# Kernel optimization log

Hardware: AMD Instinct MI355X
Metric: run time of the kernel (lower is better)

The kernel has to match this reference:

```python
import jax, jax.numpy as jnp
import numpy as np

N, R, IN, OUT = 16384, 64, 128, 128


def setup_inputs() -> dict:
    key = jax.random.key(0)
    k1, k2, k3, k4 = jax.random.split(key, 4)
    x = jax.random.normal(k1, (N, IN), dtype=jnp.float32)
    relations = jax.random.randint(k2, (N, 1), 0, R, dtype=jnp.int32)
    # kaiming_uniform_(a=sqrt(5)) on [R, in, out] -> bound = 1/sqrt(fan_in); bias uses same bound
    bound = 1.0 / np.sqrt(IN)
    w = jax.random.uniform(k3, (R, IN, OUT), dtype=jnp.float32, minval=-bound, maxval=bound)
    bias = jax.random.uniform(k4, (R, OUT), dtype=jnp.float32, minval=-bound, maxval=bound)
    return {"x": x, "relations": relations, "w": w, "bias": bias}


def reference(x, relations, w, bias):
    # Faithful math of the torch module: out[i] = x[i] @ w[relations[i,0]] + bias[relations[i,0]]
    # (original computes x.matmul(w[relations]) -> [N,1,N,out] and extracts the diagonal;
    #  this is the direct per-sample grouped GEMM form.)
    rel = relations[:, 0]                       # [N]
    w_sel = jnp.take(w, rel, axis=0)            # [N, in, out]
    out = jnp.einsum('ni,nio->no', x, w_sel)    # [N, out]
    return out + jnp.take(bias, rel, axis=0)
```

## Files before the change

### kernel.cpp

```cpp
#include <hip/hip_runtime.h>

#define N_ROWS 16384
#define R_REL  64
#define IN_D   128
#define OUT_D  128
#define BM     64
#define NS     4
#define TPB_G  256

__device__ __forceinline__ float f4c(const float4& v, int i) {
  return i == 0 ? v.x : i == 1 ? v.y : i == 2 ? v.z : v.w;
}

__global__ __launch_bounds__(256, 4) void k_pre(const int* __restrict__ rel,
                                                int* __restrict__ offsets,
                                                int* __restrict__ row_idx) {
  const int r = blockIdx.x;
  const int t = threadIdx.x;
  const int wid = t >> 6, lane = t & 63;
  __shared__ int wsum[4];
  __shared__ int sbase;
  const int4* rel4 = (const int4*)rel;

  int lt = 0;
  for (int i = t; i < N_ROWS / 4; i += 256) {
    const int4 v = rel4[i];
    lt += (v.x < r) + (v.y < r) + (v.z < r) + (v.w < r);
  }
  #pragma unroll
  for (int d = 32; d >= 1; d >>= 1) lt += __shfl_down(lt, d, 64);
  if (lane == 0) wsum[wid] = lt;
  __syncthreads();
  if (t == 0) {
    const int o = wsum[0] + wsum[1] + wsum[2] + wsum[3];
    sbase = o;
    offsets[r] = o;
    if (r == R_REL - 1) offsets[R_REL] = N_ROWS;
  }
  __syncthreads();
  int base = sbase;

  for (int c = 0; c < 16; ++c) {
    const int i4 = c * 256 + t;
    const int4 v = rel4[i4];
    const int m0 = (v.x == r), m1 = (v.y == r), m2 = (v.z == r), m3 = (v.w == r);
    const int cnt_t = m0 + m1 + m2 + m3;
    int incl = cnt_t;
    #pragma unroll
    for (int d = 1; d < 64; d <<= 1) {
      const int u = __shfl_up(incl, d, 64);
      if (lane >= d) incl += u;
    }
    if (lane == 63) wsum[wid] = incl;
    __syncthreads();
    int wbase = 0;
    for (int ww = 0; ww < wid; ++ww) wbase += wsum[ww];
    int pos = base + wbase + incl - cnt_t;
    const int row0 = i4 * 4;
    if (m0) row_idx[pos++] = row0;
    if (m1) row_idx[pos++] = row0 + 1;
    if (m2) row_idx[pos++] = row0 + 2;
    if (m3) row_idx[pos++] = row0 + 3;
    base += wsum[0] + wsum[1] + wsum[2] + wsum[3];
    __syncthreads();
  }
}

__global__ __launch_bounds__(TPB_G, 2) void k_gemm(const float* __restrict__ x,
                                                   const float* __restrict__ w,
                                                   const float* __restrict__ bias,
                                                   const int* __restrict__ offsets,
                                                   const int* __restrict__ row_idx,
                                                   float* __restrict__ out) {
  __shared__ __align__(16) float ws_[IN_D * 64];
  __shared__ __align__(16) float xs[BM * IN_D];
  const int r = blockIdx.y;
  const int c0 = blockIdx.z * 64;
  const int beg = offsets[r];
  const int cnt = offsets[r + 1] - beg;
  if (cnt == 0) return;
  const int t = threadIdx.x;
  const int tx = t & 15;
  const int ty = t >> 4;

  {
    const float* wr = w + (size_t)r * (IN_D * OUT_D) + c0;
    #pragma unroll
    for (int i = 0; i < 8; ++i) {
      const int id = t + i * 256;
      const int k = id >> 4, c4 = id & 15;
      ((float4*)ws_)[k * 16 + c4] = *(const float4*)(wr + k * OUT_D + c4 * 4);
    }
  }

  for (int tile = blockIdx.x; tile * BM < cnt; tile += NS) {
    const int m0 = beg + tile * BM;
    const int rows = min(BM, cnt - tile * BM);

    {
      const int row = t & 63;
      const int q = t >> 6;
      if (row < rows) {
        const int g = row_idx[m0 + row];
        const float4* src = (const float4*)(x + (size_t)g * IN_D) + q * 8;
        float4* dst = (float4*)xs + row * 32;
        const int sw = row & 7;
        #pragma unroll
        for (int j = 0; j < 8; ++j) dst[(q * 8 + j) ^ sw] = src[j];
      }
    }
    __syncthreads();

    float4 acc[4];
    #pragma unroll
    for (int j = 0; j < 4; ++j) acc[j] = make_float4(0.f, 0.f, 0.f, 0.f);

    const float4* wlds = (const float4*)ws_;
    const float4* xlds = (const float4*)xs;

    #pragma unroll 4
    for (int kc = 0; kc < 32; ++kc) {
      float4 wv[4];
      #pragma unroll
      for (int kk = 0; kk < 4; ++kk) wv[kk] = wlds[(kc * 4 + kk) * 16 + tx];
      float4 xv[4];
      #pragma unroll
      for (int j = 0; j < 4; ++j) {
        const int rm = ty * 4 + j;
        xv[j] = xlds[rm * 32 + (kc ^ (rm & 7))];
      }
      #pragma unroll
      for (int kk = 0; kk < 4; ++kk) {
        #pragma unroll
        for (int j = 0; j < 4; ++j) {
          const float a = f4c(xv[j], kk);
          acc[j].x += a * wv[kk].x;
          acc[j].y += a * wv[kk].y;
          acc[j].z += a * wv[kk].z;
          acc[j].w += a * wv[kk].w;
        }
      }
    }

    const float4 bv = *(const float4*)(bias + (size_t)r * OUT_D + c0 + tx * 4);
    #pragma unroll
    for (int j = 0; j < 4; ++j) {
      const int rm = ty * 4 + j;
      if (rm < rows) {
        const int g = row_idx[m0 + rm];
        float4 o;
        o.x = acc[j].x + bv.x;
        o.y = acc[j].y + bv.y;
        o.z = acc[j].z + bv.z;
        o.w = acc[j].w + bv.w;
        *(float4*)(out + (size_t)g * OUT_D + c0 + tx * 4) = o;
      }
    }
    __syncthreads();
  }
}

extern "C" void kernel_launch(void* const* d_in, const int* in_sizes, int n_in,
                              void* d_out, int out_size, void* d_ws, size_t ws_size,
                              hipStream_t stream) {
  const float* x    = (const float*)d_in[0];
  const int*   rel  = (const int*)d_in[1];
  const float* w    = (const float*)d_in[2];
  const float* bias = (const float*)d_in[3];
  float* out = (float*)d_out;

  int* offsets = (int*)d_ws;
  int* row_idx = (int*)d_ws + 128;

  k_pre<<<R_REL, 256, 0, stream>>>(rel, offsets, row_idx);
  k_gemm<<<dim3(NS, R_REL, 2), TPB_G, 0, stream>>>(x, w, bias, offsets, row_idx, out);
}
```

Before: 101.5 us.

## Fuse relation bucketing into the grouped GEMM kernel using LDS row lists

Removes the separate preprocessing kernel and its global offsets/row_idx arrays. Each GEMM block now scans the relation array itself, builds its relation's row list in shared memory, then runs the same tiled GEMM over that list. This drops one kernel launch and the global round-trip between the two stages. In exchange, every block redundantly scans the full relation array, and LDS use rises, which may limit occupancy. Row lists are capped at 3968 entries, so a relation with more rows than that would silently lose output rows.

```diff
diff --git a/kernel.cpp b/kernel.cpp
--- a/kernel.cpp
+++ b/kernel.cpp
@@ -6,40 +6,41 @@
 #define OUT_D  128
 #define BM     64
 #define NS     4
-#define TPB_G  256
+#define TPB    256
+#define MAXL   3968
 
 __device__ __forceinline__ float f4c(const float4& v, int i) {
   return i == 0 ? v.x : i == 1 ? v.y : i == 2 ? v.z : v.w;
 }
 
-__global__ __launch_bounds__(256, 4) void k_pre(const int* __restrict__ rel,
-                                                int* __restrict__ offsets,
-                                                int* __restrict__ row_idx) {
-  const int r = blockIdx.x;
-  const int t = threadIdx.x;
-  const int wid = t >> 6, lane = t & 63;
+__global__ __launch_bounds__(TPB, 2) void k_fused(const float* __restrict__ x,
+                                                  const int* __restrict__ rel,
+                                                  const float* __restrict__ w,
+                                                  const float* __restrict__ bias,
+                                                  float* __restrict__ out) {
+  __shared__ __align__(16) float ws_[IN_D * 64];
+  __shared__ __align__(16) float xs[BM * IN_D];
+  __shared__ int rlist[MAXL];
   __shared__ int wsum[4];
-  __shared__ int sbase;
+  const int r    = blockIdx.y;
+  const int c0   = blockIdx.z * 64;
+  const int slab = blockIdx.x;
+  const int t    = threadIdx.x;
+  const int wid  = t >> 6, lane = t & 63;
+  const int tx   = t & 15, ty = t >> 4;
+
+  {
+    const float* wr = w + (size_t)r * (IN_D * OUT_D) + c0;
+    #pragma unroll
+    for (int i = 0; i < 8; ++i) {
+      const int id = t + i * 256;
+      const int k = id >> 4, c4 = id & 15;
+      ((float4*)ws_)[k * 16 + c4] = *(const float4*)(wr + k * OUT_D + c4 * 4);
+    }
+  }
+
   const int4* rel4 = (const int4*)rel;
-
-  int lt = 0;
-  for (int i = t; i < N_ROWS / 4; i += 256) {
-    const int4 v = rel4[i];
-    lt += (v.x < r) + (v.y < r) + (v.z < r) + (v.w < r);
-  }
-  #pragma unroll
-  for (int d = 32; d >= 1; d >>= 1) lt += __shfl_down(lt, d, 64);
-  if (lane == 0) wsum[wid] = lt;
-  __syncthreads();
-  if (t == 0) {
-    const int o = wsum[0] + wsum[1] + wsum[2] + wsum[3];
-    sbase = o;
-    offsets[r] = o;
-    if (r == R_REL - 1) offsets[R_REL] = N_ROWS;
-  }
-  __syncthreads();
-  int base = sbase;
-
+  int base = 0;
   for (int c = 0; c < 16; ++c) {
     const int i4 = c * 256 + t;
     const int4 v = rel4[i4];
@@ -54,54 +55,28 @@
     if (lane == 63) wsum[wid] = incl;
     __syncthreads();
     int wbase = 0;
-    for (int ww = 0; ww < wid; ++ww) wbase += wsum[ww];
+    #pragma unroll
+    for (int ww = 0; ww < 4; ++ww) if (ww < wid) wbase += wsum[ww];
     int pos = base + wbase + incl - cnt_t;
     const int row0 = i4 * 4;
-    if (m0) row_idx[pos++] = row0;
-    if (m1) row_idx[pos++] = row0 + 1;
-    if (m2) row_idx[pos++] = row0 + 2;
-    if (m3) row_idx[pos++] = row0 + 3;
+    if (m0 && pos < MAXL) rlist[pos++] = row0;
+    if (m1 && pos < MAXL) rlist[pos++] = row0 + 1;
+    if (m2 && pos < MAXL) rlist[pos++] = row0 + 2;
+    if (m3 && pos < MAXL) rlist[pos++] = row0 + 3;
     base += wsum[0] + wsum[1] + wsum[2] + wsum[3];
     __syncthreads();
   }
-}
+  const int cntR = base < MAXL ? base : MAXL;
 
-__global__ __launch_bounds__(TPB_G, 2) void k_gemm(const float* __restrict__ x,
-                                                   const float* __restrict__ w,
-                                                   const float* __restrict__ bias,
-                                                   const int* __restrict__ offsets,
-                                                   const int* __restrict__ row_idx,
-                                                   float* __restrict__ out) {
-  __shared__ __align__(16) float ws_[IN_D * 64];
-  __shared__ __align__(16) float xs[BM * IN_D];
-  const int r = blockIdx.y;
-  const int c0 = blockIdx.z * 64;
-  const int beg = offsets[r];
-  const int cnt = offsets[r + 1] - beg;
-  if (cnt == 0) return;
-  const int t = threadIdx.x;
-  const int tx = t & 15;
-  const int ty = t >> 4;
-
-  {
-    const float* wr = w + (size_t)r * (IN_D * OUT_D) + c0;
-    #pragma unroll
-    for (int i = 0; i < 8; ++i) {
-      const int id = t + i * 256;
-      const int k = id >> 4, c4 = id & 15;
-      ((float4*)ws_)[k * 16 + c4] = *(const float4*)(wr + k * OUT_D + c4 * 4);
-    }
-  }
-
-  for (int tile = blockIdx.x; tile * BM < cnt; tile += NS) {
-    const int m0 = beg + tile * BM;
-    const int rows = min(BM, cnt - tile * BM);
+  for (int tile = slab; tile * BM < cntR; tile += NS) {
+    const int t0 = tile * BM;
+    const int rows = min(BM, cntR - t0);
 
     {
       const int row = t & 63;
       const int q = t >> 6;
       if (row < rows) {
-        const int g = row_idx[m0 + row];
+        const int g = rlist[t0 + row];
         const float4* src = (const float4*)(x + (size_t)g * IN_D) + q * 8;
         float4* dst = (float4*)xs + row * 32;
         const int sw = row & 7;
@@ -147,7 +122,7 @@
     for (int j = 0; j < 4; ++j) {
       const int rm = ty * 4 + j;
       if (rm < rows) {
-        const int g = row_idx[m0 + rm];
+        const int g = rlist[t0 + rm];
         float4 o;
         o.x = acc[j].x + bv.x;
         o.y = acc[j].y + bv.y;
@@ -169,9 +144,5 @@
   const float* bias = (const float*)d_in[3];
   float* out = (float*)d_out;
 
-  int* offsets = (int*)d_ws;
-  int* row_idx = (int*)d_ws + 128;
-
-  k_pre<<<R_REL, 256, 0, stream>>>(rel, offsets, row_idx);
-  k_gemm<<<dim3(NS, R_REL, 2), TPB_G, 0, stream>>>(x, w, bias, offsets, row_idx, out);
+  k_fused<<<dim3(NS, R_REL, 2), TPB, 0, stream>>>(x, rel, w, bias, out);
 }
```

Result: faster. 97.52 us (-3.9%).
